# Performance work log

Measured on AMD Instinct MI355X. Metric: run time of the kernel, lower is better.

Reference implementation:

```python
import jax, jax.numpy as jnp
import numpy as np

QUANTIZE = 20  # number of histogram bins (init arg quantize=20.0)


def setup_inputs() -> dict:
    key = jax.random.key(0)
    B, L = 64, 1_000_000
    output_seg = jax.random.uniform(key, (B, L), dtype=jnp.float32)  # scores in [0,1)
    return {"output_seg": output_seg}


def reference(output_seg) -> jnp.ndarray:
    # output_seg: [B, L] float scores in [0, 1)
    B, L = output_seg.shape
    Q = QUANTIZE
    # torch.floor(A / (1/quantize)) == floor(A * quantize)
    bins = jnp.floor(output_seg * Q).astype(jnp.int32)          # [B, L], values 0..Q-1 for x in [0,1)
    # Per-sample histogram via a single segment_sum over flattened (sample, bin) ids.
    flat_ids = (jnp.arange(B, dtype=jnp.int32)[:, None] * Q + bins).ravel()  # [B*L]
    counts = jax.ops.segment_sum(
        jnp.ones((B * L,), dtype=jnp.float32), flat_ids, num_segments=B * Q
    ).reshape(B, Q)                                              # [B, Q]
    prob = counts / jnp.float32(L)                               # [B, Q]
    # Entropy contribution only where prob != 0 (matches `if prob != 0` guard).
    safe = jnp.maximum(prob, jnp.float32(1e-30))
    ent = jnp.where(prob > 0, -prob * (jnp.log(safe) / jnp.log(jnp.float32(2.0))), jnp.float32(0.0))
    # loss accumulates over all samples (outer loop over batch sums entropies)
    return jnp.sum(ent)
```

## Files before the change

### kernel.cpp

```cpp
#include <hip/hip_runtime.h>

#define Q 20
#define REPLICAS 64
#define RSTRIDE 21
#define BLOCK 256
#define BLOCKS_PER_ROW 32
#define L_FIXED 1000000

__global__ void zero_ws_kernel(unsigned int* __restrict__ ws, int n) {
    int i = blockIdx.x * blockDim.x + threadIdx.x;
    if (i < n) ws[i] = 0u;
}

__global__ __launch_bounds__(BLOCK) void hist_kernel(const float* __restrict__ x,
                                                     unsigned int* __restrict__ ghist,
                                                     int L) {
    __shared__ unsigned int sh[REPLICAS * RSTRIDE];
    __shared__ unsigned int fin[Q];

    for (int i = threadIdx.x; i < REPLICAS * RSTRIDE; i += BLOCK) sh[i] = 0u;
    if (threadIdx.x < Q) fin[threadIdx.x] = 0u;
    __syncthreads();

    const int row = blockIdx.x / BLOCKS_PER_ROW;
    const int cb  = blockIdx.x % BLOCKS_PER_ROW;
    const float4* __restrict__ rowp = (const float4*)(x + (long long)row * L);
    const int nvec = L >> 2;
    unsigned int* myrep = sh + (threadIdx.x & (REPLICAS - 1)) * RSTRIDE;

    for (int i = cb * BLOCK + threadIdx.x; i < nvec; i += BLOCKS_PER_ROW * BLOCK) {
        float4 v = rowp[i];
        int b0 = min((int)(v.x * 20.0f), Q - 1);
        int b1 = min((int)(v.y * 20.0f), Q - 1);
        int b2 = min((int)(v.z * 20.0f), Q - 1);
        int b3 = min((int)(v.w * 20.0f), Q - 1);
        atomicAdd(&myrep[b0], 1u);
        atomicAdd(&myrep[b1], 1u);
        atomicAdd(&myrep[b2], 1u);
        atomicAdd(&myrep[b3], 1u);
    }
    __syncthreads();

    if (threadIdx.x < Q * 8) {
        int q = threadIdx.x >> 3;
        int g = threadIdx.x & 7;
        unsigned int s = 0;
        #pragma unroll
        for (int r = 0; r < 8; ++r) s += sh[(g * 8 + r) * RSTRIDE + q];
        atomicAdd(&fin[q], s);
    }
    __syncthreads();
    if (threadIdx.x < Q) atomicAdd(&ghist[row * Q + threadIdx.x], fin[threadIdx.x]);
}

__global__ __launch_bounds__(BLOCK) void entropy_kernel(const unsigned int* __restrict__ ghist,
                                                        float* __restrict__ out,
                                                        int nbins, float invL) {
    float s = 0.0f;
    for (int i = threadIdx.x; i < nbins; i += BLOCK) {
        unsigned int c = ghist[i];
        if (c > 0u) {
            float p = (float)c * invL;
            s -= p * __log2f(p);
        }
    }
    #pragma unroll
    for (int off = 32; off > 0; off >>= 1) s += __shfl_down(s, off, 64);
    __shared__ float wsum[BLOCK / 64];
    int wid  = threadIdx.x >> 6;
    int lane = threadIdx.x & 63;
    if (lane == 0) wsum[wid] = s;
    __syncthreads();
    if (threadIdx.x == 0) {
        float t = 0.0f;
        #pragma unroll
        for (int w = 0; w < BLOCK / 64; ++w) t += wsum[w];
        out[0] = t;
    }
}

extern "C" void kernel_launch(void* const* d_in, const int* in_sizes, int n_in,
                              void* d_out, int out_size, void* d_ws, size_t ws_size,
                              hipStream_t stream) {
    const float* x = (const float*)d_in[0];
    float* out = (float*)d_out;
    unsigned int* ghist = (unsigned int*)d_ws;

    const int L = L_FIXED;
    const int B = in_sizes[0] / L;
    const int nbins = B * Q;

    zero_ws_kernel<<<(nbins + BLOCK - 1) / BLOCK, BLOCK, 0, stream>>>(ghist, nbins);
    hist_kernel<<<B * BLOCKS_PER_ROW, BLOCK, 0, stream>>>(x, ghist, L);
    entropy_kernel<<<1, BLOCK, 0, stream>>>(ghist, out, nbins, 1.0f / (float)L);
}
```

Baseline: 342.5 us.

## Use per-thread LDS histograms, dual-stream loads, and drop zeroing kernel

```diff
diff --git a/kernel.cpp b/kernel.cpp
--- a/kernel.cpp
+++ b/kernel.cpp
@@ -1,43 +1,40 @@
 #include <hip/hip_runtime.h>
 
 #define Q 20
-#define REPLICAS 64
 #define RSTRIDE 21
 #define BLOCK 256
-#define BLOCKS_PER_ROW 32
+#define BLOCKS_PER_ROW 28
 #define L_FIXED 1000000
 
-__global__ void zero_ws_kernel(unsigned int* __restrict__ ws, int n) {
-    int i = blockIdx.x * blockDim.x + threadIdx.x;
-    if (i < n) ws[i] = 0u;
-}
-
 __global__ __launch_bounds__(BLOCK) void hist_kernel(const float* __restrict__ x,
-                                                     unsigned int* __restrict__ ghist,
-                                                     int L) {
-    __shared__ unsigned int sh[REPLICAS * RSTRIDE];
+                                                     unsigned int* __restrict__ part) {
+    __shared__ unsigned int sh[BLOCK * RSTRIDE];
     __shared__ unsigned int fin[Q];
 
-    for (int i = threadIdx.x; i < REPLICAS * RSTRIDE; i += BLOCK) sh[i] = 0u;
+    #pragma unroll
+    for (int i = 0; i < RSTRIDE; ++i) sh[threadIdx.x * RSTRIDE + i] = 0u;
     if (threadIdx.x < Q) fin[threadIdx.x] = 0u;
     __syncthreads();
 
     const int row = blockIdx.x / BLOCKS_PER_ROW;
     const int cb  = blockIdx.x % BLOCKS_PER_ROW;
-    const float4* __restrict__ rowp = (const float4*)(x + (long long)row * L);
-    const int nvec = L >> 2;
-    unsigned int* myrep = sh + (threadIdx.x & (REPLICAS - 1)) * RSTRIDE;
+    const float4* __restrict__ rowp = (const float4*)(x + (long long)row * L_FIXED);
+    const int nvec = L_FIXED >> 2;
+    const int half = nvec >> 1;
+    const int stride = BLOCKS_PER_ROW * BLOCK;
+    unsigned int* myrep = sh + threadIdx.x * RSTRIDE;
 
-    for (int i = cb * BLOCK + threadIdx.x; i < nvec; i += BLOCKS_PER_ROW * BLOCK) {
-        float4 v = rowp[i];
-        int b0 = min((int)(v.x * 20.0f), Q - 1);
-        int b1 = min((int)(v.y * 20.0f), Q - 1);
-        int b2 = min((int)(v.z * 20.0f), Q - 1);
-        int b3 = min((int)(v.w * 20.0f), Q - 1);
-        atomicAdd(&myrep[b0], 1u);
-        atomicAdd(&myrep[b1], 1u);
-        atomicAdd(&myrep[b2], 1u);
-        atomicAdd(&myrep[b3], 1u);
+    for (int i = cb * BLOCK + threadIdx.x; i < half; i += stride) {
+        float4 v0 = rowp[i];
+        float4 v1 = rowp[i + half];
+        int a0 = (int)(v0.x * 20.0f), a1 = (int)(v0.y * 20.0f);
+        int a2 = (int)(v0.z * 20.0f), a3 = (int)(v0.w * 20.0f);
+        int b0 = (int)(v1.x * 20.0f), b1 = (int)(v1.y * 20.0f);
+        int b2 = (int)(v1.z * 20.0f), b3 = (int)(v1.w * 20.0f);
+        atomicAdd(&myrep[a0], 1u); atomicAdd(&myrep[a1], 1u);
+        atomicAdd(&myrep[a2], 1u); atomicAdd(&myrep[a3], 1u);
+        atomicAdd(&myrep[b0], 1u); atomicAdd(&myrep[b1], 1u);
+        atomicAdd(&myrep[b2], 1u); atomicAdd(&myrep[b3], 1u);
     }
     __syncthreads();
 
@@ -46,27 +43,33 @@
         int g = threadIdx.x & 7;
         unsigned int s = 0;
         #pragma unroll
-        for (int r = 0; r < 8; ++r) s += sh[(g * 8 + r) * RSTRIDE + q];
+        for (int r = 0; r < 32; ++r) s += sh[(g * 32 + r) * RSTRIDE + q];
         atomicAdd(&fin[q], s);
     }
     __syncthreads();
-    if (threadIdx.x < Q) atomicAdd(&ghist[row * Q + threadIdx.x], fin[threadIdx.x]);
+    if (threadIdx.x < Q) part[blockIdx.x * Q + threadIdx.x] = fin[threadIdx.x];
 }
 
-__global__ __launch_bounds__(BLOCK) void entropy_kernel(const unsigned int* __restrict__ ghist,
-                                                        float* __restrict__ out,
-                                                        int nbins, float invL) {
+__global__ __launch_bounds__(1024) void entropy_kernel(const unsigned int* __restrict__ part,
+                                                       float* __restrict__ out,
+                                                       int nrows, float invL) {
     float s = 0.0f;
-    for (int i = threadIdx.x; i < nbins; i += BLOCK) {
-        unsigned int c = ghist[i];
+    const int npairs = nrows * Q;
+    for (int p = threadIdx.x; p < npairs; p += 1024) {
+        int row = p / Q;
+        int q   = p % Q;
+        unsigned int c = 0;
+        #pragma unroll
+        for (int cb = 0; cb < BLOCKS_PER_ROW; ++cb)
+            c += part[(row * BLOCKS_PER_ROW + cb) * Q + q];
         if (c > 0u) {
-            float p = (float)c * invL;
-            s -= p * __log2f(p);
+            float pr = (float)c * invL;
+            s -= pr * __log2f(pr);
         }
     }
     #pragma unroll
     for (int off = 32; off > 0; off >>= 1) s += __shfl_down(s, off, 64);
-    __shared__ float wsum[BLOCK / 64];
+    __shared__ float wsum[1024 / 64];
     int wid  = threadIdx.x >> 6;
     int lane = threadIdx.x & 63;
     if (lane == 0) wsum[wid] = s;
@@ -74,7 +77,7 @@
     if (threadIdx.x == 0) {
         float t = 0.0f;
         #pragma unroll
-        for (int w = 0; w < BLOCK / 64; ++w) t += wsum[w];
+        for (int w = 0; w < 1024 / 64; ++w) t += wsum[w];
         out[0] = t;
     }
 }
@@ -84,13 +87,10 @@
                               hipStream_t stream) {
     const float* x = (const float*)d_in[0];
     float* out = (float*)d_out;
-    unsigned int* ghist = (unsigned int*)d_ws;
+    unsigned int* part = (unsigned int*)d_ws;
 
-    const int L = L_FIXED;
-    const int B = in_sizes[0] / L;
-    const int nbins = B * Q;
+    const int B = in_sizes[0] / L_FIXED;
 
-    zero_ws_kernel<<<(nbins + BLOCK - 1) / BLOCK, BLOCK, 0, stream>>>(ghist, nbins);
-    hist_kernel<<<B * BLOCKS_PER_ROW, BLOCK, 0, stream>>>(x, ghist, L);
-    entropy_kernel<<<1, BLOCK, 0, stream>>>(ghist, out, nbins, 1.0f / (float)L);
+    hist_kernel<<<B * BLOCKS_PER_ROW, BLOCK, 0, stream>>>(x, part);
+    entropy_kernel<<<1, 1024, 0, stream>>>(part, out, B, 1.0f / (float)L_FIXED);
 }
```

Result: no change. 345.5 us, median of 2 (+0.9%).
